# Performance work log

Hardware: AMD Instinct MI355X
Metric: run time of the kernel (lower is better)

Reference implementation:

```python
import jax, jax.numpy as jnp
import numpy as np

N = 5000
NFEAT = 512
NHID = 64
NHEADS = 8
NCLASS = 40
ALPHA = 0.2  # leaky relu slope
NEG_INF = -9e15


def setup_inputs() -> dict:
    key = jax.random.key(0)
    ks = jax.random.split(key, 12)
    x = jax.random.normal(ks[0], (N, NFEAT), dtype=jnp.float32)
    # binary adjacency, ~32 avg degree, with self loops
    adj = (jax.random.uniform(ks[1], (N, N)) < (32.0 / N)).astype(jnp.float32)
    adj = jnp.maximum(adj, jnp.eye(N, dtype=jnp.float32))
    s = 1.0 / np.sqrt(NFEAT)
    W_h = jax.random.uniform(ks[2], (NHEADS, NFEAT, NHID), minval=-s, maxval=s, dtype=jnp.float32)
    a_h = jax.random.uniform(ks[3], (NHEADS, 2 * NHID), minval=-s, maxval=s, dtype=jnp.float32)
    s2 = 1.0 / np.sqrt(NHID * NHEADS)
    W_o = jax.random.uniform(ks[4], (NHID * NHEADS, NHID), minval=-s2, maxval=s2, dtype=jnp.float32)
    a_o = jax.random.uniform(ks[5], (2 * NHID,), minval=-s2, maxval=s2, dtype=jnp.float32)
    s3 = 1.0 / np.sqrt(NHID)
    fc1_w = jax.random.uniform(ks[6], (NHID, 200), minval=-s3, maxval=s3, dtype=jnp.float32)
    fc1_b = jax.random.uniform(ks[7], (200,), minval=-s3, maxval=s3, dtype=jnp.float32)
    s4 = 1.0 / np.sqrt(200)
    fc2_w = jax.random.uniform(ks[8], (200, NCLASS), minval=-s4, maxval=s4, dtype=jnp.float32)
    fc2_b = jax.random.uniform(ks[9], (NCLASS,), minval=-s4, maxval=s4, dtype=jnp.float32)
    return {"x": x, "adj": adj, "W_h": W_h, "a_h": a_h, "W_o": W_o, "a_o": a_o,
            "fc1_w": fc1_w, "fc1_b": fc1_b, "fc2_w": fc2_w, "fc2_b": fc2_b}


def _masked_attention(e, adj):
    # e: [..., N, N]; mask where adj == 0, then row softmax
    e = jnp.where(adj > 0, e, NEG_INF)
    return jax.nn.softmax(e, axis=-1)


def reference(x, adj, W_h, a_h, W_o, a_o, fc1_w, fc1_b, fc2_w, fc2_b):
    # ---- multi-head GAT layer (concat=True), eval mode (dropout off) ----
    Wh = jnp.einsum('nf,hfo->hno', x, W_h)                 # [H, N, nhid]
    f1 = jnp.einsum('hno,ho->hn', Wh, a_h[:, :NHID])       # [H, N]
    f2 = jnp.einsum('hno,ho->hn', Wh, a_h[:, NHID:])       # [H, N]
    e = jax.nn.leaky_relu(f1[:, :, None] + f2[:, None, :], ALPHA)  # [H, N, N]
    att = _masked_attention(e, adj[None, :, :])
    h = jnp.einsum('hnm,hmo->hno', att, Wh)                # [H, N, nhid]
    h1 = jax.nn.elu(h).transpose(1, 0, 2).reshape(N, NHEADS * NHID)  # concat heads

    # ---- output GAT layer (concat=False) ----
    Wh2 = h1 @ W_o                                         # [N, nhid]
    g1 = Wh2 @ a_o[:NHID]                                  # [N]
    g2 = Wh2 @ a_o[NHID:]                                  # [N]
    e2 = jax.nn.leaky_relu(g1[:, None] + g2[None, :], ALPHA)
    att2 = _masked_attention(e2, adj)
    h2 = att2 @ Wh2                                        # [N, nhid]

    # ---- MLP head ----
    h3 = jax.nn.elu(h2 @ fc1_w + fc1_b)
    return h3 @ fc2_w + fc2_b                              # [N, nclass]
```

## Files before the change

### kernel.cpp

```cpp
#include <hip/hip_runtime.h>

typedef unsigned short u16;
typedef unsigned int u32;
typedef unsigned long long u64;
typedef __bf16 bf16_t;
typedef __bf16 bf16x8 __attribute__((ext_vector_type(8)));
typedef u16 u16x8 __attribute__((ext_vector_type(8)));
typedef float f32x4 __attribute__((ext_vector_type(4)));
typedef u32 u32x4 __attribute__((ext_vector_type(4)));

#define NN 5000
#define NF 512
#define NH 64
#define HEADS 8
#define NCLS 40
#define CAP 128
#define LRELU 0.2f

#define BM_BLKS 1250
#define G1_BLKS (79 * HEADS)
#define PRM_BLKS 8
#define K1_GRID (BM_BLKS + G1_BLKS + PRM_BLKS)

__device__ __forceinline__ bool adj_is_bf16(const void* adj) {
    return ((*(const u32*)adj) & 0xFFFFu) != 0u;
}
__device__ __forceinline__ float up_bf16(u16 h) {
    return __uint_as_float((u32)h << 16);
}
__device__ __forceinline__ float in_f32(const void* p, int idx, bool isb) {
    return isb ? up_bf16(((const u16*)p)[idx]) : ((const float*)p)[idx];
}
__device__ __forceinline__ u32x4 ntload4(const void* p, int idx) {
    return __builtin_nontemporal_load(((const u32x4*)p) + idx);
}
union U8cast { u16x8 u; bf16x8 b; };

__global__ __launch_bounds__(256) void gemm1_f(const void* __restrict__ x,
                                               const void* __restrict__ W_h,
                                               const void* __restrict__ a_h,
                                               const void* __restrict__ adj,
                                               const void* W_o, const void* a_o,
                                               const void* f1w, const void* f1b,
                                               const void* f2w, const void* f2b,
                                               int* __restrict__ nbr, int* __restrict__ deg,
                                               float* __restrict__ Wh,
                                               float* __restrict__ f1,
                                               float* __restrict__ f2,
                                               float* W_oc, float* a_oc,
                                               float* f1wc, float* f1bc,
                                               float* f2wc, float* f2bc) {
    const bool isb = adj_is_bf16(adj);
    const int lane = threadIdx.x & 63;
    const int wid  = threadIdx.x >> 6;
    const int b = blockIdx.x;

    if (b < BM_BLKS) {
        const int r = b * 4 + wid;
        u64 my0 = 0ull, my1 = 0ull;
        if (!isb) {
            const float* row = (const float*)adj + (size_t)r * NN;
            #pragma unroll
            for (int pass = 0; pass < 2; ++pass) {
                u32x4 v[10];
                #pragma unroll
                for (int k = 0; k < 10; ++k) {
                    int c = (pass * 10 + k) * 64 + lane;
                    v[k] = (c < 1250) ? ntload4(row, c) : (u32x4){0u, 0u, 0u, 0u};
                }
                #pragma unroll
                for (int k = 0; k < 10; ++k) {
                    int i = pass * 10 + k;
                    #pragma unroll
                    for (int j = 0; j < 4; ++j) {
                        u64 m = __ballot(v[k][j] != 0u);
                        int w = i * 4 + j;
                        if (w == lane)      my0 = m;
                        if (w == lane + 64) my1 = m;
                    }
                }
            }
        } else {
            const u16* row = (const u16*)adj + (size_t)r * NN;
            u32x4 v[10];
            #pragma unroll
            for (int k = 0; k < 10; ++k) {
                int c = k * 64 + lane;
                v[k] = (c < 625) ? ntload4(row, c) : (u32x4){0u, 0u, 0u, 0u};
            }
            #pragma unroll
            for (int k = 0; k < 10; ++k) {
                #pragma unroll
                for (int j = 0; j < 4; ++j) {
                    u64 mlo = __ballot((v[k][j] & 0xFFFFu) != 0u);
                    u64 mhi = __ballot((v[k][j] >> 16) != 0u);
                    int wl = k * 8 + 2 * j, wh = wl + 1;
                    if (wl == lane)      my0 = mlo;
                    if (wl == lane + 64) my1 = mlo;
                    if (wh == lane)      my0 = mhi;
                    if (wh == lane + 64) my1 = mhi;
                }
            }
        }
        int* nrow = nbr + (size_t)r * CAP;
        int pc = __popcll(my0);
        int scan = pc;
        #pragma unroll
        for (int o = 1; o < 64; o <<= 1) {
            int t2 = __shfl_up(scan, o);
            if (lane >= o) scan += t2;
        }
        int off = scan - pc;
        {
            const int w = lane;
            u64 mw = my0;
            while (mw) {
                int bb = __ffsll(mw) - 1;
                mw &= mw - 1;
                int elem = !isb ? ((w >> 2) * 64 + bb) * 4 + (w & 3)
                                : ((w >> 3) * 64 + bb) * 8 + (w & 7);
                if (off < CAP) nrow[off] = elem;
                ++off;
            }
        }
        const int base = __shfl(scan, 63);
        int pc1 = __popcll(my1);
        int scan1 = pc1;
        #pragma unroll
        for (int o = 1; o < 64; o <<= 1) {
            int t2 = __shfl_up(scan1, o);
            if (lane >= o) scan1 += t2;
        }
        int off1 = base + scan1 - pc1;
        {
            const int w = lane + 64;
            u64 mw = my1;
            while (mw) {
                int bb = __ffsll(mw) - 1;
                mw &= mw - 1;
                int elem = !isb ? ((w >> 2) * 64 + bb) * 4 + (w & 3)
                                : ((w >> 3) * 64 + bb) * 8 + (w & 7);
                if (off1 < CAP) nrow[off1] = elem;
                ++off1;
            }
        }
        const int total = base + __shfl(scan1, 63);
        if (lane == 0) deg[r] = total < CAP ? total : CAP;
        return;
    }

    if (b >= BM_BLKS + G1_BLKS) {
        const int s1 = HEADS * NH * NH, s2 = 2 * NH,
                  s3 = NH * 200, s4 = 200, s5 = 200 * NCLS, s6 = NCLS;
        const int total = s1 + s2 + s3 + s4 + s5 + s6;
        const int pb = b - (BM_BLKS + G1_BLKS);
        for (int i = pb * 256 + threadIdx.x; i < total; i += PRM_BLKS * 256) {
            const void* src; float* dst; int off = i;
            if (off < s1) { src = W_o;  dst = W_oc; }
            else if ((off -= s1) < s2) { src = a_o;  dst = a_oc; }
            else if ((off -= s2) < s3) { src = f1w;  dst = f1wc; }
            else if ((off -= s3) < s4) { src = f1b;  dst = f1bc; }
            else if ((off -= s4) < s5) { src = f2w;  dst = f2wc; }
            else { off -= s5;           src = f2b;  dst = f2bc; }
            dst[off] = isb ? up_bf16(((const u16*)src)[off]) : ((const float*)src)[off];
        }
        return;
    }

    const int g = b - BM_BLKS;
    const int rg = g % 79;
    const int h  = g / 79;
    const int quad = lane >> 4;
    const int lr   = lane & 15;
    const int kq   = quad * 8;
    const int nCol = wid * 16 + lr;
    __shared__ float f1s[4][64], f2s[4][64];

    bf16x8 bfrag[16];
    if (!isb) {
        const float* Bh = (const float*)W_h + (size_t)h * NF * NH;
        #pragma unroll
        for (int s = 0; s < 16; ++s) {
            bf16x8 bb;
            #pragma unroll
            for (int j = 0; j < 8; ++j) bb[j] = (bf16_t)Bh[(s * 32 + kq + j) * NH + nCol];
            bfrag[s] = bb;
        }
    } else {
        const u16* Bh = (const u16*)W_h + (size_t)h * NF * NH;
        #pragma unroll
        for (int s = 0; s < 16; ++s) {
            U8cast cc;
            #pragma unroll
            for (int j = 0; j < 8; ++j) cc.u[j] = Bh[(s * 32 + kq + j) * NH + nCol];
            bfrag[s] = cc.b;
        }
    }
    const float a1c = in_f32(a_h, h * 128 + nCol, isb);
    const float a2c = in_f32(a_h, h * 128 + NH + nCol, isb);

    for (int t = 0; t < 4; ++t) {
        const int rb = rg * 64 + t * 16;
        int row  = rb + lr;
        int rowc = row < NN ? row : NN - 1;
        f32x4 acc = {0.f, 0.f, 0.f, 0.f};
        if (!isb) {
            const float* xp = (const float*)x + (size_t)rowc * NF + kq;
            #pragma unroll
            for (int s = 0; s < 16; ++s) {
                float4 lo = *(const float4*)(xp + s * 32);
                float4 hi = *(const float4*)(xp + s * 32 + 4);
                bf16x8 a;
                a[0] = (bf16_t)lo.x; a[1] = (bf16_t)lo.y; a[2] = (bf16_t)lo.z; a[3] = (bf16_t)lo.w;
                a[4] = (bf16_t)hi.x; a[5] = (bf16_t)hi.y; a[6] = (bf16_t)hi.z; a[7] = (bf16_t)hi.w;
                acc = __builtin_amdgcn_mfma_f32_16x16x32_bf16(a, bfrag[s], acc, 0, 0, 0);
            }
        } else {
            const u16* xp = (const u16*)x + (size_t)rowc * NF + kq;
            #pragma unroll
            for (int s = 0; s < 16; ++s) {
                U8cast cc;
                cc.u = *(const u16x8*)(xp + s * 32);
                acc = __builtin_amdgcn_mfma_f32_16x16x32_bf16(cc.b, bfrag[s], acc, 0, 0, 0);
            }
        }
        #pragma unroll
        for (int r = 0; r < 4; ++r) {
            int gr = rb + quad * 4 + r;
            if (gr < NN) Wh[(size_t)gr * (HEADS * NH) + h * NH + nCol] = acc[r];
            float p1 = acc[r] * a1c, p2 = acc[r] * a2c;
            #pragma unroll
            for (int o = 8; o; o >>= 1) { p1 += __shfl_xor(p1, o); p2 += __shfl_xor(p2, o); }
            if (lr == 0) { f1s[wid][t * 16 + quad * 4 + r] = p1; f2s[wid][t * 16 + quad * 4 + r] = p2; }
        }
    }
    __syncthreads();
    if (wid == 0) {
        int gr = rg * 64 + lane;
        if (gr < NN) {
            f1[h * NN + gr] = f1s[0][lane] + f1s[1][lane] + f1s[2][lane] + f1s[3][lane];
            f2[h * NN + gr] = f2s[0][lane] + f2s[1][lane] + f2s[2][lane] + f2s[3][lane];
        }
    }
}

__global__ __launch_bounds__(256) void agg1f(const int* __restrict__ nbr,
                                             const int* __restrict__ deg,
                                             const float* __restrict__ Wh,
                                             const float* __restrict__ f1,
                                             const float* __restrict__ f2,
                                             float* __restrict__ h1) {
    const int lane = threadIdx.x & 63;
    const int wid  = threadIdx.x >> 6;
    const int n = blockIdx.x;
    __shared__ int s_nbr[CAP];
    __shared__ float s_p[8][CAP];
    const int d = deg[n];
    for (int i = threadIdx.x; i < d; i += 256) s_nbr[i] = nbr[(size_t)n * CAP + i];
    __syncthreads();

    const int ha = wid, hb = wid + 4;
    const int nb0 = (lane < d) ? s_nbr[lane] : 0;
    const int nb1 = (lane + 64 < d) ? s_nbr[lane + 64] : 0;
    const float f10 = f1[ha * NN + n], f11 = f1[hb * NN + n];
    const float* f2ha = f2 + (size_t)ha * NN;
    const float* f2hb = f2 + (size_t)hb * NN;

    float e00 = -INFINITY, e01 = -INFINITY, e10 = -INFINITY, e11 = -INFINITY;
    if (lane < d) {
        float a = f10 + f2ha[nb0]; e00 = a > 0.f ? a : LRELU * a;
        float b = f11 + f2hb[nb0]; e10 = b > 0.f ? b : LRELU * b;
    }
    if (lane + 64 < d) {
        float a = f10 + f2ha[nb1]; e01 = a > 0.f ? a : LRELU * a;
        float b = f11 + f2hb[nb1]; e11 = b > 0.f ? b : LRELU * b;
    }
    float mx0 = fmaxf(e00, e01), mx1 = fmaxf(e10, e11);
    #pragma unroll
    for (int o = 32; o; o >>= 1) {
        mx0 = fmaxf(mx0, __shfl_xor(mx0, o));
        mx1 = fmaxf(mx1, __shfl_xor(mx1, o));
    }
    float p00 = lane < d ? expf(e00 - mx0) : 0.f;
    float p01 = lane + 64 < d ? expf(e01 - mx0) : 0.f;
    float p10 = lane < d ? expf(e10 - mx1) : 0.f;
    float p11 = lane + 64 < d ? expf(e11 - mx1) : 0.f;
    float sm0 = p00 + p01, sm1 = p10 + p11;
    #pragma unroll
    for (int o = 32; o; o >>= 1) { sm0 += __shfl_xor(sm0, o); sm1 += __shfl_xor(sm1, o); }

    const float i0 = 1.f / sm0, i1 = 1.f / sm1;
    s_p[ha][lane] = p00 * i0; s_p[ha][lane + 64] = p01 * i0;
    s_p[hb][lane] = p10 * i1; s_p[hb][lane + 64] = p11 * i1;
    __syncthreads();

    const float* ap = s_p[2 * wid + (lane >> 5)];
    const float* wp = Wh + wid * 128 + 2 * lane;
    float A0x = 0.f, A0y = 0.f, A1x = 0.f, A1y = 0.f;
    float A2x = 0.f, A2y = 0.f, A3x = 0.f, A3y = 0.f;
    int j = 0;
    for (; j + 8 <= d; j += 8) {
        #pragma unroll
        for (int u = 0; u < 8; ++u) {
            const float2 v = *(const float2*)(wp + (size_t)s_nbr[j + u] * (HEADS * NH));
            const float a = ap[j + u];
            if ((u & 3) == 0)      { A0x += a * v.x; A0y += a * v.y; }
            else if ((u & 3) == 1) { A1x += a * v.x; A1y += a * v.y; }
            else if ((u & 3) == 2) { A2x += a * v.x; A2y += a * v.y; }
            else                   { A3x += a * v.x; A3y += a * v.y; }
        }
    }
    for (; j < d; ++j) {
        const float2 v = *(const float2*)(wp + (size_t)s_nbr[j] * (HEADS * NH));
        const float a = ap[j];
        A0x += a * v.x; A0y += a * v.y;
    }
    float hx = A0x + A1x + A2x + A3x;
    float hy = A0y + A1y + A2y + A3y;
    hx = hx > 0.f ? hx : expf(hx) - 1.f;
    hy = hy > 0.f ? hy : expf(hy) - 1.f;
    *(float2*)(h1 + (size_t)n * (HEADS * NH) + wid * 128 + 2 * lane) = make_float2(hx, hy);
}

__global__ __launch_bounds__(256) void gemm2_4(const float* __restrict__ h1,
                                               const float* __restrict__ W_o,
                                               const float* __restrict__ a_o,
                                               float* __restrict__ Wh2,
                                               float* __restrict__ g1,
                                               float* __restrict__ g2) {
    const int t = threadIdx.x;
    const int n0 = blockIdx.x * 4;
    __shared__ float sh[4 * 512];
    __shared__ float ps[4][4][64];
    const float4* src = (const float4*)(h1 + (size_t)n0 * 512);
    ((float4*)sh)[t]       = src[t];
    ((float4*)sh)[t + 256] = src[t + 256];
    __syncthreads();
    const int o = t & 63, part = t >> 6;
    float a0 = 0.f, a1 = 0.f, a2 = 0.f, a3 = 0.f;
    const float* wo = W_o + part * 128 * 64 + o;
    const float* s0 = sh + part * 128;
    #pragma unroll 4
    for (int f = 0; f < 128; ++f) {
        float w = wo[f * 64];
        a0 += s0[f] * w; a1 += s0[512 + f] * w; a2 += s0[1024 + f] * w; a3 += s0[1536 + f] * w;
    }
    ps[part][0][o] = a0; ps[part][1][o] = a1; ps[part][2][o] = a2; ps[part][3][o] = a3;
    __syncthreads();
    const int nd = t >> 6;
    float w2 = ps[0][nd][o] + ps[1][nd][o] + ps[2][nd][o] + ps[3][nd][o];
    Wh2[(size_t)(n0 + nd) * 64 + o] = w2;
    float p1 = w2 * a_o[o], p2 = w2 * a_o[64 + o];
    #pragma unroll
    for (int s = 32; s; s >>= 1) { p1 += __shfl_xor(p1, s); p2 += __shfl_xor(p2, s); }
    if (o == 0) { g1[n0 + nd] = p1; g2[n0 + nd] = p2; }
}

__global__ __launch_bounds__(256) void agg2_mlp(const float* __restrict__ Wh2,
                                                const float* __restrict__ g1,
                                                const float* __restrict__ g2,
                                                const int* __restrict__ nbr,
                                                const int* __restrict__ deg,
                                                const float* __restrict__ fc1_w,
                                                const float* __restrict__ fc1_b,
                                                const float* __restrict__ fc2_w,
                                                const float* __restrict__ fc2_b,
                                                float* __restrict__ out) {
    const int lane = threadIdx.x & 63;
    const int wid  = threadIdx.x >> 6;
    const int t = threadIdx.x;
    const int n0 = blockIdx.x * 4;
    const int n = n0 + wid;
    __shared__ float s_alpha[4][CAP];
    __shared__ int   s_nbr[4][CAP];
    __shared__ float s_h2[4][NH];
    __shared__ float s_h3[4][200];
    __shared__ float ps2[2][4][NCLS];
    const int d = deg[n];
    const int* nb = nbr + (size_t)n * CAP;
    const float gn = g1[n];

    float mx = -INFINITY;
    for (int j = lane; j < d; j += 64) {
        int m = nb[j];
        s_nbr[wid][j] = m;
        float e = gn + g2[m];
        e = e > 0.f ? e : LRELU * e;
        s_alpha[wid][j] = e;
        mx = fmaxf(mx, e);
    }
    #pragma unroll
    for (int o = 32; o; o >>= 1) mx = fmaxf(mx, __shfl_xor(mx, o));
    float sm = 0.f;
    for (int j = lane; j < d; j += 64) {
        float p = expf(s_alpha[wid][j] - mx);
        s_alpha[wid][j] = p;
        sm += p;
    }
    #pragma unroll
    for (int o = 32; o; o >>= 1) sm += __shfl_xor(sm, o);

    float acc0 = 0.f, acc1 = 0.f, acc2 = 0.f, acc3 = 0.f;
    int j = 0;
    for (; j + 4 <= d; j += 4) {
        acc0 += s_alpha[wid][j]     * Wh2[(size_t)s_nbr[wid][j]     * NH + lane];
        acc1 += s_alpha[wid][j + 1] * Wh2[(size_t)s_nbr[wid][j + 1] * NH + lane];
        acc2 += s_alpha[wid][j + 2] * Wh2[(size_t)s_nbr[wid][j + 2] * NH + lane];
        acc3 += s_alpha[wid][j + 3] * Wh2[(size_t)s_nbr[wid][j + 3] * NH + lane];
    }
    for (; j < d; ++j) acc0 += s_alpha[wid][j] * Wh2[(size_t)s_nbr[wid][j] * NH + lane];
    s_h2[wid][lane] = (acc0 + acc1 + acc2 + acc3) / sm;
    __syncthreads();

    if (t < 200) {
        float b0 = 0.f, b1 = 0.f, b2 = 0.f, b3 = 0.f;
        #pragma unroll 4
        for (int f = 0; f < NH; ++f) {
            float w = fc1_w[f * 200 + t];
            b0 += s_h2[0][f] * w; b1 += s_h2[1][f] * w; b2 += s_h2[2][f] * w; b3 += s_h2[3][f] * w;
        }
        float bb = fc1_b[t];
        b0 += bb; b1 += bb; b2 += bb; b3 += bb;
        s_h3[0][t] = b0 > 0.f ? b0 : expf(b0) - 1.f;
        s_h3[1][t] = b1 > 0.f ? b1 : expf(b1) - 1.f;
        s_h3[2][t] = b2 > 0.f ? b2 : expf(b2) - 1.f;
        s_h3[3][t] = b3 > 0.f ? b3 : expf(b3) - 1.f;
    }
    __syncthreads();

    if (t < 80) {
        const int o = t % 40, fh = t / 40;
        float c0 = 0.f, c1 = 0.f, c2 = 0.f, c3 = 0.f;
        #pragma unroll 4
        for (int f = fh * 100; f < fh * 100 + 100; ++f) {
            float w = fc2_w[f * NCLS + o];
            c0 += s_h3[0][f] * w; c1 += s_h3[1][f] * w; c2 += s_h3[2][f] * w; c3 += s_h3[3][f] * w;
        }
        ps2[fh][0][o] = c0; ps2[fh][1][o] = c1; ps2[fh][2][o] = c2; ps2[fh][3][o] = c3;
    }
    __syncthreads();
    if (t < 160) {
        const int nd = t / 40, o = t % 40;
        out[(size_t)(n0 + nd) * NCLS + o] = ps2[0][nd][o] + ps2[1][nd][o] + fc2_b[o];
    }
}

extern "C" void kernel_launch(void* const* d_in, const int* in_sizes, int n_in,
                              void* d_out, int out_size, void* d_ws, size_t ws_size,
                              hipStream_t stream) {
    const void* x     = d_in[0];
    const void* adj   = d_in[1];
    const void* W_h   = d_in[2];
    const void* a_h   = d_in[3];
    const void* W_o   = d_in[4];
    const void* a_o   = d_in[5];
    const void* fc1_w = d_in[6];
    const void* fc1_b = d_in[7];
    const void* fc2_w = d_in[8];
    const void* fc2_b = d_in[9];
    float* out = (float*)d_out;

    char* ws = (char*)d_ws;
    int*   nbr   = (int*)(ws + 0);
    int*   deg   = (int*)(ws + 2560000);
    float* Wh    = (float*)(ws + 2580000);
    float* f1    = (float*)(ws + 12820000);
    float* f2    = (float*)(ws + 12980000);
    float* h1    = (float*)(ws + 13140000);
    float* Wh2   = (float*)(ws + 23380000);
    float* g1    = (float*)(ws + 24660000);
    float* g2    = (float*)(ws + 24680000);
    float* W_oc  = (float*)(ws + 24700000);
    float* a_oc  = (float*)(ws + 24831072);
    float* f1wc  = (float*)(ws + 24831584);
    float* f1bc  = (float*)(ws + 24882784);
    float* f2wc  = (float*)(ws + 24883584);
    float* f2bc  = (float*)(ws + 24915584);

    gemm1_f<<<K1_GRID, 256, 0, stream>>>(x, W_h, a_h, adj,
                                         W_o, a_o, fc1_w, fc1_b, fc2_w, fc2_b,
                                         nbr, deg, Wh, f1, f2,
                                         W_oc, a_oc, f1wc, f1bc, f2wc, f2bc);
    agg1f<<<NN, 256, 0, stream>>>(nbr, deg, Wh, f1, f2, h1);
    gemm2_4<<<NN / 4, 256, 0, stream>>>(h1, W_oc, a_oc, Wh2, g1, g2);
    agg2_mlp<<<NN / 4, 256, 0, stream>>>(Wh2, g1, g2, nbr, deg,
                                         f1wc, f1bc, f2wc, f2bc, out);
}
```

Baseline: 286.8 us.

## Pre-swizzle W_h into MFMA fragment layout and interleave adjacency and GEMM blocks

A new pre-kernel converts W_h to bf16 once and stores it in the exact per-lane MFMA B-fragment order, so each GEMM1 block loads its fragments with contiguous 16-byte loads. Before, every one of the 632 GEMM blocks did 128 strided scalar loads and conversions. The parameter-copy blocks move into the new kernel, and the first kernel now interleaves adjacency-scan blocks with GEMM blocks in a 2:1 pattern to balance memory-bound and compute-bound work. The cost is an extra kernel launch and a small extra workspace write and read.

```diff
diff --git a/kernel.cpp b/kernel.cpp
--- a/kernel.cpp
+++ b/kernel.cpp
@@ -19,12 +19,19 @@
 
 #define BM_BLKS 1250
 #define G1_BLKS (79 * HEADS)
+#define K1_GRID (BM_BLKS + G1_BLKS)
+#define W0_BLKS 64
 #define PRM_BLKS 8
-#define K1_GRID (BM_BLKS + G1_BLKS + PRM_BLKS)
+#define K0_GRID (W0_BLKS + PRM_BLKS)
 
 __device__ __forceinline__ bool adj_is_bf16(const void* adj) {
     return ((*(const u32*)adj) & 0xFFFFu) != 0u;
 }
+__device__ __forceinline__ u16 rne_bf16(float f) {
+    u32 u = __float_as_uint(f);
+    u += 0x7FFFu + ((u >> 16) & 1u);
+    return (u16)(u >> 16);
+}
 __device__ __forceinline__ float up_bf16(u16 h) {
     return __uint_as_float((u32)h << 16);
 }
@@ -36,27 +43,82 @@
 }
 union U8cast { u16x8 u; bf16x8 b; };
 
+__global__ __launch_bounds__(256) void cvt_w(const void* __restrict__ W_h,
+                                             const void* __restrict__ adj,
+                                             const void* W_o, const void* a_o,
+                                             const void* f1w, const void* f1b,
+                                             const void* f2w, const void* f2b,
+                                             u16* __restrict__ whc,
+                                             float* W_oc, float* a_oc,
+                                             float* f1wc, float* f1bc,
+                                             float* f2wc, float* f2bc) {
+    const bool isb = adj_is_bf16(adj);
+    const int b = blockIdx.x;
+    if (b < W0_BLKS) {
+        const int W4 = HEADS * NF * NH / 4;
+        for (int iw = b * 256 + threadIdx.x; iw < W4; iw += W0_BLKS * 256) {
+            u16 q[4];
+            if (isb) {
+                ushort4 vv = ((const ushort4*)W_h)[iw];
+                q[0] = vv.x; q[1] = vv.y; q[2] = vv.z; q[3] = vv.w;
+            } else {
+                u32x4 vv = ntload4(W_h, iw);
+                q[0] = rne_bf16(__uint_as_float(vv[0])); q[1] = rne_bf16(__uint_as_float(vv[1]));
+                q[2] = rne_bf16(__uint_as_float(vv[2])); q[3] = rne_bf16(__uint_as_float(vv[3]));
+            }
+            const int e0 = iw * 4;
+            const int h = e0 >> 15;
+            const int rem = e0 & 32767;
+            const int f = rem >> 6, o0 = rem & 63;
+            const int base = (h * 16 + (f >> 5)) * 2048 + ((f >> 3) & 3) * 128 + (f & 7);
+            #pragma unroll
+            for (int k = 0; k < 4; ++k) {
+                const int o = o0 + k;
+                whc[base + (o >> 4) * 512 + (o & 15) * 8] = q[k];
+            }
+        }
+    } else {
+        const int s1 = HEADS * NH * NH, s2 = 2 * NH,
+                  s3 = NH * 200, s4 = 200, s5 = 200 * NCLS, s6 = NCLS;
+        const int total = s1 + s2 + s3 + s4 + s5 + s6;
+        const int pb = b - W0_BLKS;
+        for (int i = pb * 256 + threadIdx.x; i < total; i += PRM_BLKS * 256) {
+            const void* src; float* dst; int off = i;
+            if (off < s1) { src = W_o;  dst = W_oc; }
+            else if ((off -= s1) < s2) { src = a_o;  dst = a_oc; }
+            else if ((off -= s2) < s3) { src = f1w;  dst = f1wc; }
+            else if ((off -= s3) < s4) { src = f1b;  dst = f1bc; }
+            else if ((off -= s4) < s5) { src = f2w;  dst = f2wc; }
+            else { off -= s5;           src = f2b;  dst = f2bc; }
+            dst[off] = isb ? up_bf16(((const u16*)src)[off]) : ((const float*)src)[off];
+        }
+    }
+}
+
 __global__ __launch_bounds__(256) void gemm1_f(const void* __restrict__ x,
-                                               const void* __restrict__ W_h,
+                                               const bf16_t* __restrict__ Wf,
                                                const void* __restrict__ a_h,
                                                const void* __restrict__ adj,
-                                               const void* W_o, const void* a_o,
-                                               const void* f1w, const void* f1b,
-                                               const void* f2w, const void* f2b,
                                                int* __restrict__ nbr, int* __restrict__ deg,
                                                float* __restrict__ Wh,
                                                float* __restrict__ f1,
-                                               float* __restrict__ f2,
-                                               float* W_oc, float* a_oc,
-                                               float* f1wc, float* f1bc,
-                                               float* f2wc, float* f2bc) {
+                                               float* __restrict__ f2) {
     const bool isb = adj_is_bf16(adj);
     const int lane = threadIdx.x & 63;
     const int wid  = threadIdx.x >> 6;
     const int b = blockIdx.x;
 
-    if (b < BM_BLKS) {
-        const int r = b * 4 + wid;
+    int aidx = -1, gidx = -1;
+    if (b < 1875) {
+        const int g = b / 3, r3 = b % 3;
+        if (r3 < 2) aidx = 2 * g + r3;
+        else        gidx = g;
+    } else {
+        gidx = 625 + (b - 1875);
+    }
+
+    if (aidx >= 0) {
+        const int r = aidx * 4 + wid;
         u64 my0 = 0ull, my1 = 0ull;
         if (!isb) {
             const float* row = (const float*)adj + (size_t)r * NN;
@@ -149,53 +211,19 @@
         return;
     }
 
-    if (b >= BM_BLKS + G1_BLKS) {
-        const int s1 = HEADS * NH * NH, s2 = 2 * NH,
-                  s3 = NH * 200, s4 = 200, s5 = 200 * NCLS, s6 = NCLS;
-        const int total = s1 + s2 + s3 + s4 + s5 + s6;
-        const int pb = b - (BM_BLKS + G1_BLKS);
-        for (int i = pb * 256 + threadIdx.x; i < total; i += PRM_BLKS * 256) {
-            const void* src; float* dst; int off = i;
-            if (off < s1) { src = W_o;  dst = W_oc; }
-            else if ((off -= s1) < s2) { src = a_o;  dst = a_oc; }
-            else if ((off -= s2) < s3) { src = f1w;  dst = f1wc; }
-            else if ((off -= s3) < s4) { src = f1b;  dst = f1bc; }
-            else if ((off -= s4) < s5) { src = f2w;  dst = f2wc; }
-            else { off -= s5;           src = f2b;  dst = f2bc; }
-            dst[off] = isb ? up_bf16(((const u16*)src)[off]) : ((const float*)src)[off];
-        }
-        return;
-    }
-
-    const int g = b - BM_BLKS;
-    const int rg = g % 79;
-    const int h  = g / 79;
+    const int rg = gidx % 79;
+    const int h  = gidx / 79;
     const int quad = lane >> 4;
     const int lr   = lane & 15;
     const int kq   = quad * 8;
     const int nCol = wid * 16 + lr;
     __shared__ float f1s[4][64], f2s[4][64];
 
+    const bf16_t* Bf = Wf + (size_t)h * (16 * 2048) + threadIdx.x * 8;
     bf16x8 bfrag[16];
-    if (!isb) {
-        const float* Bh = (const float*)W_h + (size_t)h * NF * NH;
-        #pragma unroll
-        for (int s = 0; s < 16; ++s) {
-            bf16x8 bb;
-            #pragma unroll
-            for (int j = 0; j < 8; ++j) bb[j] = (bf16_t)Bh[(s * 32 + kq + j) * NH + nCol];
-            bfrag[s] = bb;
-        }
-    } else {
-        const u16* Bh = (const u16*)W_h + (size_t)h * NF * NH;
-        #pragma unroll
-        for (int s = 0; s < 16; ++s) {
-            U8cast cc;
-            #pragma unroll
-            for (int j = 0; j < 8; ++j) cc.u[j] = Bh[(s * 32 + kq + j) * NH + nCol];
-            bfrag[s] = cc.b;
-        }
-    }
+    #pragma unroll
+    for (int s = 0; s < 16; ++s) bfrag[s] = *(const bf16x8*)(Bf + s * 2048);
+
     const float a1c = in_f32(a_h, h * 128 + nCol, isb);
     const float a2c = in_f32(a_h, h * 128 + NH + nCol, isb);
 
@@ -476,11 +504,12 @@
     float* f1bc  = (float*)(ws + 24882784);
     float* f2wc  = (float*)(ws + 24883584);
     float* f2bc  = (float*)(ws + 24915584);
-
-    gemm1_f<<<K1_GRID, 256, 0, stream>>>(x, W_h, a_h, adj,
-                                         W_o, a_o, fc1_w, fc1_b, fc2_w, fc2_b,
-                                         nbr, deg, Wh, f1, f2,
-                                         W_oc, a_oc, f1wc, f1bc, f2wc, f2bc);
+    u16*   whc   = (u16*)(ws + 24915744);
+
+    cvt_w<<<K0_GRID, 256, 0, stream>>>(W_h, adj, W_o, a_o, fc1_w, fc1_b, fc2_w, fc2_b,
+                                       whc, W_oc, a_oc, f1wc, f1bc, f2wc, f2bc);
+    gemm1_f<<<K1_GRID, 256, 0, stream>>>(x, (const bf16_t*)whc, a_h, adj,
+                                         nbr, deg, Wh, f1, f2);
     agg1f<<<NN, 256, 0, stream>>>(nbr, deg, Wh, f1, f2, h1);
     gemm2_4<<<NN / 4, 256, 0, stream>>>(h1, W_oc, a_oc, Wh2, g1, g2);
     agg2_mlp<<<NN / 4, 256, 0, stream>>>(Wh2, g1, g2, nbr, deg,
```

Measured after the change: 301.8 us. +5.2%, slower.
